# Kernel optimization log

Hardware: AMD Instinct MI355X
Metric: run time of the kernel (lower is better)

The kernel has to match this reference:

```python
import jax, jax.numpy as jnp
import numpy as np

D_MODEL = 512
WINDOW_SIZE = 257


def setup_inputs() -> dict:
    key = jax.random.key(0)
    ks = jax.random.split(key, 7)
    B, S, D = 4, 4096, D_MODEL
    scale = 1.0 / np.sqrt(D)
    return {
        "x": jax.random.normal(ks[0], (B, S, D), dtype=jnp.float32),
        "Wq": jax.random.normal(ks[1], (D, D), dtype=jnp.float32) * scale,
        "bq": jnp.zeros((D,), dtype=jnp.float32),
        "Wk": jax.random.normal(ks[2], (D, D), dtype=jnp.float32) * scale,
        "bk": jnp.zeros((D,), dtype=jnp.float32),
        "Wv": jax.random.normal(ks[3], (D, D), dtype=jnp.float32) * scale,
        "bv": jnp.zeros((D,), dtype=jnp.float32),
    }


def reference(x, Wq, bq, Wk, bk, Wv, bv):
    B, S, D = x.shape
    half_window = (WINDOW_SIZE - 1) // 2
    Q = x @ Wq + bq
    K = x @ Wk + bk
    V = x @ Wv + bv
    # full [B,S,S] scores, then band mask |i-j| <= half_window (matches original)
    scores = jnp.einsum("bsd,btd->bst", Q, K) / jnp.sqrt(jnp.asarray(D, x.dtype))
    idx = jnp.arange(S)
    local_mask = jnp.abs(idx[:, None] - idx[None, :]) <= half_window  # [S,S]
    scores = jnp.where(local_mask[None], scores, -jnp.inf)
    attn = jax.nn.softmax(scores, axis=-1)
    return jnp.einsum("bst,btd->bsd", attn, V)
```

## Files before the change

kernel.cpp:

```cpp
#include <hip/hip_runtime.h>
#include <hip/hip_bf16.h>

#define S_LEN   4096
#define D_MOD   512
#define BATCH   4
#define HALF_W  128
#define M_TOT   (BATCH * S_LEN)

typedef __attribute__((ext_vector_type(8))) short bf16x8;
typedef __attribute__((ext_vector_type(4))) float f32x4;

__device__ __forceinline__ unsigned short f2bf(float f) {
    unsigned int u = __float_as_uint(f);
    unsigned int r = (u + 0x7fffu + ((u >> 16) & 1u)) >> 16;
    return (unsigned short)r;
}

__device__ __forceinline__ void async_copy16(const void* g, void* l) {
    __builtin_amdgcn_global_load_lds(
        (const __attribute__((address_space(1))) void*)g,
        (__attribute__((address_space(3))) void*)l, 16, 0, 0);
}

__global__ __launch_bounds__(256) void convert_xw(const float* __restrict__ x,
                                                  const float* __restrict__ Wq,
                                                  const float* __restrict__ Wk,
                                                  const float* __restrict__ Wv,
                                                  unsigned short* __restrict__ xb,
                                                  unsigned short* __restrict__ Wt) {
    __shared__ float sT[64][65];
    const int t = threadIdx.x;
    const int bid = blockIdx.x;
    if (bid < 8192) {
        int i = (bid * 256 + t) * 4;
        float4 v = *(const float4*)(x + i);
        ushort4 o;
        o.x = f2bf(v.x); o.y = f2bf(v.y); o.z = f2bf(v.z); o.w = f2bf(v.w);
        *(ushort4*)(xb + i) = o;
        return;
    }
    const int j = bid - 8192;
    const int w = j >> 6;
    const int rj = j & 63;
    const float* W = (w == 0) ? Wq : ((w == 1) ? Wk : Wv);
    const int n0 = (rj & 7) * 64, k0 = (rj >> 3) * 64;
    const int r = t >> 4, c4 = (t & 15) * 4;
    #pragma unroll
    for (int i = 0; i < 4; ++i) {
        float4 v = *(const float4*)(W + (size_t)(k0 + r + i * 16) * 512 + n0 + c4);
        sT[c4 + 0][r + i * 16] = v.x;
        sT[c4 + 1][r + i * 16] = v.y;
        sT[c4 + 2][r + i * 16] = v.z;
        sT[c4 + 3][r + i * 16] = v.w;
    }
    __syncthreads();
    #pragma unroll
    for (int i = 0; i < 4; ++i) {
        int rr = (t >> 4) + i * 16;
        ushort4 o;
        o.x = f2bf(sT[rr][c4 + 0]);
        o.y = f2bf(sT[rr][c4 + 1]);
        o.z = f2bf(sT[rr][c4 + 2]);
        o.w = f2bf(sT[rr][c4 + 3]);
        *(ushort4*)(Wt + (size_t)w * 262144 + (size_t)(n0 + rr) * 512 + k0 + c4) = o;
    }
}

__global__ __launch_bounds__(256) void qkv_gemm(
    const unsigned short* __restrict__ xb, const unsigned short* __restrict__ Wt,
    const float* __restrict__ bq, const float* __restrict__ bk, const float* __restrict__ bv,
    unsigned short* __restrict__ Qo, unsigned short* __restrict__ Ko,
    unsigned short* __restrict__ Vt) {
    __shared__ __align__(16) char gsmem[34816];
    unsigned short* sA = (unsigned short*)gsmem;
    unsigned short* sB = (unsigned short*)(gsmem + 16384);
    unsigned short* sT = (unsigned short*)gsmem;

    const int t = threadIdx.x;
    const int p = blockIdx.x;
    const int l = (p & 7) * 192 + (p >> 3);
    const int mi = l / 12;
    const int rzn = l - mi * 12;
    const int wsel = rzn >> 2;
    const int ni = rzn & 3;
    const int m0 = mi * 128;
    const int n0 = ni * 128;
    const unsigned short* Wb = Wt + (size_t)wsel * 262144;

    const int w = t >> 6, lane = t & 63;
    const int wm = (w & 1) * 64, wn = (w >> 1) * 64;
    const int qd = lane >> 4, l16 = lane & 15;

    f32x4 acc[4][4] = {};

    for (int k0 = 0; k0 < 512; k0 += 64) {
        __syncthreads();
        #pragma unroll
        for (int i = 0; i < 4; ++i) {
            int c = i * 256 + t;
            int row = c >> 3, cc = c & 7;
            int g = cc ^ (row & 7);
            async_copy16(xb + (size_t)(m0 + row) * 512 + k0 + g * 8, sA + c * 8);
            async_copy16(Wb + (size_t)(n0 + row) * 512 + k0 + g * 8, sB + c * 8);
        }
        __syncthreads();
        #pragma unroll
        for (int ks = 0; ks < 2; ++ks) {
            bf16x8 af[4], bfr[4];
            #pragma unroll
            for (int i = 0; i < 4; ++i) {
                int row = wm + i * 16 + l16;
                int ch = (ks * 4 + qd) ^ (row & 7);
                af[i] = *(const bf16x8*)(sA + row * 64 + ch * 8);
            }
            #pragma unroll
            for (int j = 0; j < 4; ++j) {
                int row = wn + j * 16 + l16;
                int ch = (ks * 4 + qd) ^ (row & 7);
                bfr[j] = *(const bf16x8*)(sB + row * 64 + ch * 8);
            }
            #pragma unroll
            for (int i = 0; i < 4; ++i)
                #pragma unroll
                for (int j = 0; j < 4; ++j)
                    acc[i][j] = __builtin_amdgcn_mfma_f32_16x16x32_bf16(af[i], bfr[j], acc[i][j], 0, 0, 0);
        }
    }

    const float* bias = (wsel == 0) ? bq : ((wsel == 1) ? bk : bv);
    __syncthreads();

    if (wsel < 2) {
        #pragma unroll
        for (int j = 0; j < 4; ++j) {
            int n = wn + j * 16 + l16;
            float bj = bias[n0 + n];
            #pragma unroll
            for (int i = 0; i < 4; ++i) {
                int mb = wm + i * 16 + qd * 4;
                #pragma unroll
                for (int r = 0; r < 4; ++r)
                    sT[(mb + r) * 136 + n] = f2bf(acc[i][j][r] + bj);
            }
        }
        __syncthreads();
        unsigned short* Og = (wsel == 0) ? Qo : Ko;
        #pragma unroll
        for (int i2 = 0; i2 < 4; ++i2)
            #pragma unroll
            for (int i3 = 0; i3 < 2; ++i3) {
                int m = i2 * 32 + (t >> 3);
                int ch = (t & 7) + i3 * 8;
                bf16x8 v = *(const bf16x8*)(sT + m * 136 + ch * 8);
                *(bf16x8*)(Og + (size_t)(m0 + m) * 512 + n0 + ch * 8) = v;
            }
    } else {
        #pragma unroll
        for (int j = 0; j < 4; ++j) {
            int n = wn + j * 16 + l16;
            float bj = bias[n0 + n];
            #pragma unroll
            for (int i = 0; i < 4; ++i) {
                int mb = wm + i * 16 + qd * 4;
                #pragma unroll
                for (int r = 0; r < 4; ++r)
                    sT[n * 136 + mb + r] = f2bf(acc[i][j][r] + bj);
            }
        }
        __syncthreads();
        #pragma unroll
        for (int i2 = 0; i2 < 4; ++i2)
            #pragma unroll
            for (int i3 = 0; i3 < 2; ++i3) {
                int n = i2 * 32 + (t >> 3);
                int ch = (t & 7) + i3 * 8;
                bf16x8 v = *(const bf16x8*)(sT + n * 136 + ch * 8);
                *(bf16x8*)(Vt + (size_t)(n0 + n) * M_TOT + m0 + ch * 8) = v;
            }
    }
}

__global__ __launch_bounds__(256) void attn(const unsigned short* __restrict__ Qg,
                                            const unsigned short* __restrict__ Kg,
                                            const unsigned short* __restrict__ Vt,
                                            float* __restrict__ out) {
    __shared__ __align__(16) unsigned short sQ[32 * 520];
    __shared__ __align__(16) unsigned short sKV[32 * 520];
    __shared__ __align__(16) unsigned short sP[32 * 40];
    __shared__ float lsum[32];

    const int t = threadIdx.x;
    const int p = blockIdx.x;
    const int l = (p & 7) * 64 + (p >> 3);
    const int q0 = (l & 127) * 32;
    const int b = l >> 7;
    const int bS = b * S_LEN;
    const int w = t >> 6, lane = t & 63;
    const int qd = lane >> 4, l16 = lane & 15;
    const int qh = (w >> 1) * 16, kh = (w & 1) * 16;

    if (t < 32) lsum[t] = 0.f;

    #pragma unroll
    for (int i = 0; i < 8; ++i) {
        int c = i * 256 + t;
        int row = c >> 6, cc = c & 63;
        async_copy16(Qg + (bS + q0 + row) * 512 + cc * 8, sQ + row * 520 + cc * 8);
    }
    asm volatile("s_waitcnt vmcnt(0)" ::: "memory");

    const int kt_lo = (q0 < 128) ? ((128 - q0) >> 5) : 0;
    int kt_hi = (4192 - q0) >> 5;
    if (kt_hi > 8) kt_hi = 8;

    bf16x8 kreg[8], vreg[8];

    {
        int key0 = q0 - HALF_W + kt_lo * 32;
        #pragma unroll
        for (int i = 0; i < 8; ++i) {
            int c = i * 256 + t;
            int row = c >> 6, cc = c & 63;
            int rowg = key0 + row;
            rowg = (rowg < 0) ? 0 : ((rowg > S_LEN - 1) ? S_LEN - 1 : rowg);
            kreg[i] = *(const bf16x8*)(Kg + (size_t)(bS + rowg) * 512 + cc * 8);
        }
    }

    f32x4 oacc[16] = {};

    for (int kt = kt_lo; kt <= kt_hi; ++kt) {
        const int key0 = q0 - HALF_W + kt * 32;

        asm volatile("s_waitcnt lgkmcnt(0)" ::: "memory");
        __builtin_amdgcn_s_barrier();

        #pragma unroll
        for (int i = 0; i < 8; ++i) {
            int c = i * 256 + t;
            int row = c >> 6, cc = c & 63;
            *(bf16x8*)(sKV + row * 520 + cc * 8) = kreg[i];
        }

        #pragma unroll
        for (int i = 0; i < 8; ++i) {
            int c = i * 256 + t;
            int rp = c >> 3, chs = c & 7;
            int ch = chs ^ (rp & 7);
            int d = rp * 2 + (ch >> 2);
            int kc = ch & 3;
            int kk = key0 + kc * 8;
            int koff = (kk >= 0 && kk + 8 <= S_LEN) ? kk : 0;
            vreg[i] = *(const bf16x8*)(Vt + (size_t)d * M_TOT + bS + koff);
        }

        asm volatile("s_waitcnt lgkmcnt(0)" ::: "memory");
        __builtin_amdgcn_s_barrier();

        f32x4 sacc = {0.f, 0.f, 0.f, 0.f};
        #pragma unroll
        for (int c4 = 0; c4 < 4; ++c4) {
            #pragma unroll
            for (int kc = 0; kc < 4; ++kc) {
                bf16x8 aq  = *(const bf16x8*)(sQ  + (qh + l16) * 520 + c4 * 128 + kc * 32 + qd * 8);
                bf16x8 bk8 = *(const bf16x8*)(sKV + (kh + l16) * 520 + c4 * 128 + kc * 32 + qd * 8);
                sacc = __builtin_amdgcn_mfma_f32_16x16x32_bf16(aq, bk8, sacc, 0, 0, 0);
            }
        }

        const float scale = 0.04419417382415922f;
        #pragma unroll
        for (int r = 0; r < 4; ++r) {
            int qi = q0 + qh + qd * 4 + r;
            int kj = key0 + kh + l16;
            bool valid = (kj >= 0) && (kj < S_LEN) && (kj >= qi - HALF_W) && (kj <= qi + HALF_W);
            float p2 = valid ? __expf(sacc[r] * scale) : 0.f;
            sP[(qh + qd * 4 + r) * 40 + kh + l16] = f2bf(p2);
            float s = p2;
            s += __shfl_xor(s, 1);
            s += __shfl_xor(s, 2);
            s += __shfl_xor(s, 4);
            s += __shfl_xor(s, 8);
            if (l16 == 0) atomicAdd(&lsum[qh + qd * 4 + r], s);
        }

        asm volatile("s_waitcnt lgkmcnt(0)" ::: "memory");
        __builtin_amdgcn_s_barrier();

        #pragma unroll
        for (int i = 0; i < 8; ++i) {
            int c = i * 256 + t;
            *(bf16x8*)(sKV + c * 8) = vreg[i];
        }

        if (kt < kt_hi) {
            int key0n = key0 + 32;
            #pragma unroll
            for (int i = 0; i < 8; ++i) {
                int c = i * 256 + t;
                int row = c >> 6, cc = c & 63;
                int rowg = key0n + row;
                rowg = (rowg < 0) ? 0 : ((rowg > S_LEN - 1) ? S_LEN - 1 : rowg);
                kreg[i] = *(const bf16x8*)(Kg + (size_t)(bS + rowg) * 512 + cc * 8);
            }
        }

        asm volatile("s_waitcnt lgkmcnt(0)" ::: "memory");
        __builtin_amdgcn_s_barrier();

        #pragma unroll
        for (int c4 = 0; c4 < 4; ++c4) {
            #pragma unroll
            for (int qt = 0; qt < 2; ++qt) {
                bf16x8 ap = *(const bf16x8*)(sP + (qt * 16 + l16) * 40 + qd * 8);
                #pragma unroll
                for (int dt = 0; dt < 2; ++dt) {
                    int dv = c4 * 128 + w * 32 + dt * 16 + l16;
                    int rp = dv >> 1;
                    int chs = (((dv & 1) << 2) + qd) ^ (rp & 7);
                    bf16x8 bv8 = *(const bf16x8*)(sKV + rp * 64 + chs * 8);
                    oacc[c4 * 4 + qt * 2 + dt] =
                        __builtin_amdgcn_mfma_f32_16x16x32_bf16(ap, bv8, oacc[c4 * 4 + qt * 2 + dt], 0, 0, 0);
                }
            }
        }
    }

    asm volatile("s_waitcnt lgkmcnt(0)" ::: "memory");
    __builtin_amdgcn_s_barrier();

    float inv[2][4];
    #pragma unroll
    for (int qt = 0; qt < 2; ++qt)
        #pragma unroll
        for (int r = 0; r < 4; ++r)
            inv[qt][r] = 1.0f / lsum[qt * 16 + qd * 4 + r];

    #pragma unroll
    for (int c4 = 0; c4 < 4; ++c4)
        #pragma unroll
        for (int qt = 0; qt < 2; ++qt)
            #pragma unroll
            for (int dt = 0; dt < 2; ++dt) {
                int dv = c4 * 128 + w * 32 + dt * 16 + l16;
                #pragma unroll
                for (int r = 0; r < 4; ++r) {
                    int q = qt * 16 + qd * 4 + r;
                    out[(size_t)(bS + q0 + q) * 512 + dv] = oacc[c4 * 4 + qt * 2 + dt][r] * inv[qt][r];
                }
            }
}

extern "C" void kernel_launch(void* const* d_in, const int* in_sizes, int n_in,
                              void* d_out, int out_size, void* d_ws, size_t ws_size,
                              hipStream_t stream) {
    const float* x  = (const float*)d_in[0];
    const float* Wq = (const float*)d_in[1];
    const float* bq = (const float*)d_in[2];
    const float* Wk = (const float*)d_in[3];
    const float* bk = (const float*)d_in[4];
    const float* Wv = (const float*)d_in[5];
    const float* bv = (const float*)d_in[6];
    float* out = (float*)d_out;

    char* ws = (char*)d_ws;
    unsigned short* xb = (unsigned short*)(ws);
    unsigned short* Wt = (unsigned short*)(ws + 16777216);
    unsigned short* Qb = (unsigned short*)(ws + 18350080);
    unsigned short* Kb = (unsigned short*)(ws + 35127296);
    unsigned short* Vt = (unsigned short*)(ws + 51904512);

    convert_xw<<<8384, 256, 0, stream>>>(x, Wq, Wk, Wv, xb, Wt);
    qkv_gemm<<<1536, 256, 0, stream>>>(xb, Wt, bq, bk, bv, Qb, Kb, Vt);
    attn<<<512, 256, 0, stream>>>(Qb, Kb, Vt, out);
}
```

Measured before the change: 165.1 us.

## Warp-specialize attention into QK-softmax and PV groups with pipelined tiles

The attention kernel grows to 512 threads. Four waves load K, compute QK^T and the exponentials, while the other four waves load V and run the P·V MFMAs on the previous key tile, using a double-buffered P buffer. Q is staged once through LDS into registers so QK^T no longer re-reads Q from shared memory, and K and V get separate LDS buffers. This aims to overlap the score and output phases and cut per-tile barriers, at the cost of higher register pressure under launch_bounds(512,2), which could spill, and an extra drain iteration per block.

```diff
diff --git a/kernel.cpp b/kernel.cpp
--- a/kernel.cpp
+++ b/kernel.cpp
@@ -180,13 +180,13 @@
     }
 }
 
-__global__ __launch_bounds__(256) void attn(const unsigned short* __restrict__ Qg,
-                                            const unsigned short* __restrict__ Kg,
-                                            const unsigned short* __restrict__ Vt,
-                                            float* __restrict__ out) {
-    __shared__ __align__(16) unsigned short sQ[32 * 520];
-    __shared__ __align__(16) unsigned short sKV[32 * 520];
-    __shared__ __align__(16) unsigned short sP[32 * 40];
+__global__ __launch_bounds__(512, 2) void attn(const unsigned short* __restrict__ Qg,
+                                               const unsigned short* __restrict__ Kg,
+                                               const unsigned short* __restrict__ Vt,
+                                               float* __restrict__ out) {
+    __shared__ __align__(16) unsigned short sK[32 * 520];
+    __shared__ __align__(16) unsigned short sV[32 * 512];
+    __shared__ __align__(16) unsigned short sP[2][32 * 40];
     __shared__ float lsum[32];
 
     const int t = threadIdx.x;
@@ -195,160 +195,192 @@
     const int q0 = (l & 127) * 32;
     const int b = l >> 7;
     const int bS = b * S_LEN;
-    const int w = t >> 6, lane = t & 63;
+
+    const bool isA = (t < 256);
+    const int ta = t & 255;
+    const int w = (t >> 6) & 3;
+    const int lane = t & 63;
     const int qd = lane >> 4, l16 = lane & 15;
     const int qh = (w >> 1) * 16, kh = (w & 1) * 16;
 
     if (t < 32) lsum[t] = 0.f;
-
-    #pragma unroll
-    for (int i = 0; i < 8; ++i) {
-        int c = i * 256 + t;
-        int row = c >> 6, cc = c & 63;
-        async_copy16(Qg + (bS + q0 + row) * 512 + cc * 8, sQ + row * 520 + cc * 8);
-    }
-    asm volatile("s_waitcnt vmcnt(0)" ::: "memory");
 
     const int kt_lo = (q0 < 128) ? ((128 - q0) >> 5) : 0;
     int kt_hi = (4192 - q0) >> 5;
     if (kt_hi > 8) kt_hi = 8;
 
-    bf16x8 kreg[8], vreg[8];
+    bf16x8 kreg[8], vreg[8], qreg[16];
+    f32x4 oacc[16] = {};
 
     {
         int key0 = q0 - HALF_W + kt_lo * 32;
-        #pragma unroll
-        for (int i = 0; i < 8; ++i) {
-            int c = i * 256 + t;
-            int row = c >> 6, cc = c & 63;
-            int rowg = key0 + row;
-            rowg = (rowg < 0) ? 0 : ((rowg > S_LEN - 1) ? S_LEN - 1 : rowg);
-            kreg[i] = *(const bf16x8*)(Kg + (size_t)(bS + rowg) * 512 + cc * 8);
-        }
-    }
-
-    f32x4 oacc[16] = {};
-
-    for (int kt = kt_lo; kt <= kt_hi; ++kt) {
+        if (isA) {
+            #pragma unroll
+            for (int i = 0; i < 8; ++i) {
+                int c = i * 256 + ta;
+                int row = c >> 6, cc = c & 63;
+                int rowg = key0 + row;
+                rowg = (rowg < 0) ? 0 : ((rowg > S_LEN - 1) ? S_LEN - 1 : rowg);
+                kreg[i] = *(const bf16x8*)(Kg + (size_t)(bS + rowg) * 512 + cc * 8);
+            }
+        } else {
+            #pragma unroll
+            for (int i = 0; i < 8; ++i) {
+                int c = i * 256 + ta;
+                int rp = c >> 3, chs = c & 7;
+                int ch = chs ^ (rp & 7);
+                int d = rp * 2 + (ch >> 2);
+                int kc = ch & 3;
+                int kk = key0 + kc * 8;
+                int koff = (kk >= 0 && kk + 8 <= S_LEN) ? kk : 0;
+                vreg[i] = *(const bf16x8*)(Vt + (size_t)d * M_TOT + bS + koff);
+            }
+        }
+    }
+
+    #pragma unroll
+    for (int i = 0; i < 4; ++i) {
+        int c = i * 512 + t;
+        int row = c >> 6, cc = c & 63;
+        async_copy16(Qg + (size_t)(bS + q0 + row) * 512 + cc * 8, sK + row * 512 + cc * 8);
+    }
+    asm volatile("s_waitcnt vmcnt(0)" ::: "memory");
+    __builtin_amdgcn_s_barrier();
+    if (isA) {
+        #pragma unroll
+        for (int c4 = 0; c4 < 4; ++c4)
+            #pragma unroll
+            for (int kc = 0; kc < 4; ++kc)
+                qreg[c4 * 4 + kc] = *(const bf16x8*)(sK + (qh + l16) * 512 + c4 * 128 + kc * 32 + qd * 8);
+    }
+    asm volatile("s_waitcnt lgkmcnt(0)" ::: "memory");
+    __builtin_amdgcn_s_barrier();
+
+    for (int kt = kt_lo; kt <= kt_hi + 1; ++kt) {
         const int key0 = q0 - HALF_W + kt * 32;
+
+        if (isA) {
+            if (kt <= kt_hi) {
+                #pragma unroll
+                for (int i = 0; i < 8; ++i) {
+                    int c = i * 256 + ta;
+                    int row = c >> 6, cc = c & 63;
+                    *(bf16x8*)(sK + row * 520 + cc * 8) = kreg[i];
+                }
+                if (kt < kt_hi) {
+                    int key0n = key0 + 32;
+                    #pragma unroll
+                    for (int i = 0; i < 8; ++i) {
+                        int c = i * 256 + ta;
+                        int row = c >> 6, cc = c & 63;
+                        int rowg = key0n + row;
+                        rowg = (rowg < 0) ? 0 : ((rowg > S_LEN - 1) ? S_LEN - 1 : rowg);
+                        kreg[i] = *(const bf16x8*)(Kg + (size_t)(bS + rowg) * 512 + cc * 8);
+                    }
+                }
+            }
+        } else {
+            if (kt > kt_lo) {
+                #pragma unroll
+                for (int i = 0; i < 8; ++i) {
+                    int c = i * 256 + ta;
+                    *(bf16x8*)(sV + c * 8) = vreg[i];
+                }
+            }
+            if (kt > kt_lo && kt <= kt_hi) {
+                #pragma unroll
+                for (int i = 0; i < 8; ++i) {
+                    int c = i * 256 + ta;
+                    int rp = c >> 3, chs = c & 7;
+                    int ch = chs ^ (rp & 7);
+                    int d = rp * 2 + (ch >> 2);
+                    int kc = ch & 3;
+                    int kk = key0 + kc * 8;
+                    int koff = (kk >= 0 && kk + 8 <= S_LEN) ? kk : 0;
+                    vreg[i] = *(const bf16x8*)(Vt + (size_t)d * M_TOT + bS + koff);
+                }
+            }
+        }
 
         asm volatile("s_waitcnt lgkmcnt(0)" ::: "memory");
         __builtin_amdgcn_s_barrier();
 
-        #pragma unroll
-        for (int i = 0; i < 8; ++i) {
-            int c = i * 256 + t;
-            int row = c >> 6, cc = c & 63;
-            *(bf16x8*)(sKV + row * 520 + cc * 8) = kreg[i];
-        }
-
-        #pragma unroll
-        for (int i = 0; i < 8; ++i) {
-            int c = i * 256 + t;
-            int rp = c >> 3, chs = c & 7;
-            int ch = chs ^ (rp & 7);
-            int d = rp * 2 + (ch >> 2);
-            int kc = ch & 3;
-            int kk = key0 + kc * 8;
-            int koff = (kk >= 0 && kk + 8 <= S_LEN) ? kk : 0;
-            vreg[i] = *(const bf16x8*)(Vt + (size_t)d * M_TOT + bS + koff);
+        if (isA) {
+            if (kt <= kt_hi) {
+                f32x4 sacc = {0.f, 0.f, 0.f, 0.f};
+                #pragma unroll
+                for (int c4 = 0; c4 < 4; ++c4) {
+                    #pragma unroll
+                    for (int kc = 0; kc < 4; ++kc) {
+                        bf16x8 bk8 = *(const bf16x8*)(sK + (kh + l16) * 520 + c4 * 128 + kc * 32 + qd * 8);
+                        sacc = __builtin_amdgcn_mfma_f32_16x16x32_bf16(qreg[c4 * 4 + kc], bk8, sacc, 0, 0, 0);
+                    }
+                }
+                const float scale = 0.04419417382415922f;
+                unsigned short* sPt = sP[kt & 1];
+                #pragma unroll
+                for (int r = 0; r < 4; ++r) {
+                    int qi = q0 + qh + qd * 4 + r;
+                    int kj = key0 + kh + l16;
+                    bool valid = (kj >= 0) && (kj < S_LEN) && (kj >= qi - HALF_W) && (kj <= qi + HALF_W);
+                    float p2 = valid ? __expf(sacc[r] * scale) : 0.f;
+                    sPt[(qh + qd * 4 + r) * 40 + kh + l16] = f2bf(p2);
+                    float s = p2;
+                    s += __shfl_xor(s, 1);
+                    s += __shfl_xor(s, 2);
+                    s += __shfl_xor(s, 4);
+                    s += __shfl_xor(s, 8);
+                    if (l16 == 0) atomicAdd(&lsum[qh + qd * 4 + r], s);
+                }
+            }
+        } else {
+            if (kt > kt_lo) {
+                const unsigned short* sPp = sP[(kt - 1) & 1];
+                #pragma unroll
+                for (int c4 = 0; c4 < 4; ++c4) {
+                    #pragma unroll
+                    for (int qt = 0; qt < 2; ++qt) {
+                        bf16x8 ap = *(const bf16x8*)(sPp + (qt * 16 + l16) * 40 + qd * 8);
+                        #pragma unroll
+                        for (int dt = 0; dt < 2; ++dt) {
+                            int dv = c4 * 128 + w * 32 + dt * 16 + l16;
+                            int rp = dv >> 1;
+                            int chs = (((dv & 1) << 2) + qd) ^ (rp & 7);
+                            bf16x8 bv8 = *(const bf16x8*)(sV + rp * 64 + chs * 8);
+                            oacc[c4 * 4 + qt * 2 + dt] =
+                                __builtin_amdgcn_mfma_f32_16x16x32_bf16(ap, bv8, oacc[c4 * 4 + qt * 2 + dt], 0, 0, 0);
+                        }
+                    }
+                }
+            }
         }
 
         asm volatile("s_waitcnt lgkmcnt(0)" ::: "memory");
         __builtin_amdgcn_s_barrier();
-
-        f32x4 sacc = {0.f, 0.f, 0.f, 0.f};
-        #pragma unroll
-        for (int c4 = 0; c4 < 4; ++c4) {
-            #pragma unroll
-            for (int kc = 0; kc < 4; ++kc) {
-                bf16x8 aq  = *(const bf16x8*)(sQ  + (qh + l16) * 520 + c4 * 128 + kc * 32 + qd * 8);
-                bf16x8 bk8 = *(const bf16x8*)(sKV + (kh + l16) * 520 + c4 * 128 + kc * 32 + qd * 8);
-                sacc = __builtin_amdgcn_mfma_f32_16x16x32_bf16(aq, bk8, sacc, 0, 0, 0);
-            }
-        }
-
-        const float scale = 0.04419417382415922f;
-        #pragma unroll
-        for (int r = 0; r < 4; ++r) {
-            int qi = q0 + qh + qd * 4 + r;
-            int kj = key0 + kh + l16;
-            bool valid = (kj >= 0) && (kj < S_LEN) && (kj >= qi - HALF_W) && (kj <= qi + HALF_W);
-            float p2 = valid ? __expf(sacc[r] * scale) : 0.f;
-            sP[(qh + qd * 4 + r) * 40 + kh + l16] = f2bf(p2);
-            float s = p2;
-            s += __shfl_xor(s, 1);
-            s += __shfl_xor(s, 2);
-            s += __shfl_xor(s, 4);
-            s += __shfl_xor(s, 8);
-            if (l16 == 0) atomicAdd(&lsum[qh + qd * 4 + r], s);
-        }
-
-        asm volatile("s_waitcnt lgkmcnt(0)" ::: "memory");
-        __builtin_amdgcn_s_barrier();
-
-        #pragma unroll
-        for (int i = 0; i < 8; ++i) {
-            int c = i * 256 + t;
-            *(bf16x8*)(sKV + c * 8) = vreg[i];
-        }
-
-        if (kt < kt_hi) {
-            int key0n = key0 + 32;
-            #pragma unroll
-            for (int i = 0; i < 8; ++i) {
-                int c = i * 256 + t;
-                int row = c >> 6, cc = c & 63;
-                int rowg = key0n + row;
-                rowg = (rowg < 0) ? 0 : ((rowg > S_LEN - 1) ? S_LEN - 1 : rowg);
-                kreg[i] = *(const bf16x8*)(Kg + (size_t)(bS + rowg) * 512 + cc * 8);
-            }
-        }
-
-        asm volatile("s_waitcnt lgkmcnt(0)" ::: "memory");
-        __builtin_amdgcn_s_barrier();
-
-        #pragma unroll
-        for (int c4 = 0; c4 < 4; ++c4) {
-            #pragma unroll
-            for (int qt = 0; qt < 2; ++qt) {
-                bf16x8 ap = *(const bf16x8*)(sP + (qt * 16 + l16) * 40 + qd * 8);
+    }
+
+    if (!isA) {
+        float inv[2][4];
+        #pragma unroll
+        for (int qt = 0; qt < 2; ++qt)
+            #pragma unroll
+            for (int r = 0; r < 4; ++r)
+                inv[qt][r] = 1.0f / lsum[qt * 16 + qd * 4 + r];
+
+        #pragma unroll
+        for (int c4 = 0; c4 < 4; ++c4)
+            #pragma unroll
+            for (int qt = 0; qt < 2; ++qt)
                 #pragma unroll
                 for (int dt = 0; dt < 2; ++dt) {
                     int dv = c4 * 128 + w * 32 + dt * 16 + l16;
-                    int rp = dv >> 1;
-                    int chs = (((dv & 1) << 2) + qd) ^ (rp & 7);
-                    bf16x8 bv8 = *(const bf16x8*)(sKV + rp * 64 + chs * 8);
-                    oacc[c4 * 4 + qt * 2 + dt] =
-                        __builtin_amdgcn_mfma_f32_16x16x32_bf16(ap, bv8, oacc[c4 * 4 + qt * 2 + dt], 0, 0, 0);
-                }
-            }
-        }
-    }
-
-    asm volatile("s_waitcnt lgkmcnt(0)" ::: "memory");
-    __builtin_amdgcn_s_barrier();
-
-    float inv[2][4];
-    #pragma unroll
-    for (int qt = 0; qt < 2; ++qt)
-        #pragma unroll
-        for (int r = 0; r < 4; ++r)
-            inv[qt][r] = 1.0f / lsum[qt * 16 + qd * 4 + r];
-
-    #pragma unroll
-    for (int c4 = 0; c4 < 4; ++c4)
-        #pragma unroll
-        for (int qt = 0; qt < 2; ++qt)
-            #pragma unroll
-            for (int dt = 0; dt < 2; ++dt) {
-                int dv = c4 * 128 + w * 32 + dt * 16 + l16;
-                #pragma unroll
-                for (int r = 0; r < 4; ++r) {
-                    int q = qt * 16 + qd * 4 + r;
-                    out[(size_t)(bS + q0 + q) * 512 + dv] = oacc[c4 * 4 + qt * 2 + dt][r] * inv[qt][r];
-                }
-            }
+                    #pragma unroll
+                    for (int r = 0; r < 4; ++r) {
+                        int q = qt * 16 + qd * 4 + r;
+                        out[(size_t)(bS + q0 + q) * 512 + dv] = oacc[c4 * 4 + qt * 2 + dt][r] * inv[qt][r];
+                    }
+                }
+    }
 }
 
 extern "C" void kernel_launch(void* const* d_in, const int* in_sizes, int n_in,
@@ -372,5 +404,5 @@
 
     convert_xw<<<8384, 256, 0, stream>>>(x, Wq, Wk, Wv, xb, Wt);
     qkv_gemm<<<1536, 256, 0, stream>>>(xb, Wt, bq, bk, bv, Qb, Kb, Vt);
-    attn<<<512, 256, 0, stream>>>(Qb, Kb, Vt, out);
-}
+    attn<<<512, 512, 0, stream>>>(Qb, Kb, Vt, out);
+}
```

After: 199.9 us. 1.21x slower.

## Double-buffer K/V tiles via async LDS loads with 64-query, 512-thread blocks

Applied to the files above, without the earlier changes.

The attention kernel moves to 64-query tiles processed by 512 threads. K and V tiles are fetched straight into LDS with global_load_lds and double-buffered, so the next tile's loads overlap the current tile's MFMAs. Q fragments are loaded once into registers from a swizzled LDS copy, which removes the repeated Q LDS reads. The block now uses about 134KB of LDS and 256 blocks, which lowers occupancy and grid parallelism and processes one extra key tile per block.

```diff
diff --git a/kernel.cpp b/kernel.cpp
--- a/kernel.cpp
+++ b/kernel.cpp
@@ -180,94 +180,128 @@
     }
 }
 
-__global__ __launch_bounds__(256) void attn(const unsigned short* __restrict__ Qg,
-                                            const unsigned short* __restrict__ Kg,
-                                            const unsigned short* __restrict__ Vt,
-                                            float* __restrict__ out) {
-    __shared__ __align__(16) unsigned short sQ[32 * 520];
-    __shared__ __align__(16) unsigned short sKV[32 * 520];
-    __shared__ __align__(16) unsigned short sP[32 * 40];
-    __shared__ float lsum[32];
+__global__ __launch_bounds__(512, 2) void attn(const unsigned short* __restrict__ Qg,
+                                               const unsigned short* __restrict__ Kg,
+                                               const unsigned short* __restrict__ Vt,
+                                               float* __restrict__ out) {
+    __shared__ __align__(16) char smem[137472];
+    unsigned short* const bK0 = (unsigned short*)(smem);
+    unsigned short* const bK1 = (unsigned short*)(smem + 66048);
+    unsigned short* const bV0 = (unsigned short*)(smem + 33280);
+    unsigned short* const bV1 = (unsigned short*)(smem + 99328);
+    unsigned short* const sQ  = (unsigned short*)(smem + 66048);
+    unsigned short* const sP  = (unsigned short*)(smem + 132096);
+    float* const lsum = (float*)(smem + 137216);
 
     const int t = threadIdx.x;
     const int p = blockIdx.x;
-    const int l = (p & 7) * 64 + (p >> 3);
-    const int q0 = (l & 127) * 32;
-    const int b = l >> 7;
+    const int l = (p & 7) * 32 + (p >> 3);
+    const int q0 = (l & 63) * 64;
+    const int b = l >> 6;
     const int bS = b * S_LEN;
+
     const int w = t >> 6, lane = t & 63;
     const int qd = lane >> 4, l16 = lane & 15;
-    const int qh = (w >> 1) * 16, kh = (w & 1) * 16;
-
-    if (t < 32) lsum[t] = 0.f;
-
-    #pragma unroll
-    for (int i = 0; i < 8; ++i) {
-        int c = i * 256 + t;
-        int row = c >> 6, cc = c & 63;
-        async_copy16(Qg + (bS + q0 + row) * 512 + cc * 8, sQ + row * 520 + cc * 8);
-    }
-    asm volatile("s_waitcnt vmcnt(0)" ::: "memory");
+    const int qs = w >> 1;
+    const int qh = qs * 16;
+    const int kh = (w & 1) * 16;
+    const int dh = (w & 1) * 256;
+
+    if (t < 64) lsum[t] = 0.f;
 
     const int kt_lo = (q0 < 128) ? ((128 - q0) >> 5) : 0;
     int kt_hi = (4192 - q0) >> 5;
-    if (kt_hi > 8) kt_hi = 8;
-
-    bf16x8 kreg[8], vreg[8];
+    if (kt_hi > 9) kt_hi = 9;
+
+    bf16x8 qreg[16];
+    f32x4 oacc[16] = {};
 
     {
         int key0 = q0 - HALF_W + kt_lo * 32;
         #pragma unroll
-        for (int i = 0; i < 8; ++i) {
-            int c = i * 256 + t;
+        for (int i = 0; i < 4; ++i) {
+            int c = i * 512 + t;
             int row = c >> 6, cc = c & 63;
             int rowg = key0 + row;
             rowg = (rowg < 0) ? 0 : ((rowg > S_LEN - 1) ? S_LEN - 1 : rowg);
-            kreg[i] = *(const bf16x8*)(Kg + (size_t)(bS + rowg) * 512 + cc * 8);
-        }
-    }
-
-    f32x4 oacc[16] = {};
-
-    for (int kt = kt_lo; kt <= kt_hi; ++kt) {
-        const int key0 = q0 - HALF_W + kt * 32;
-
-        asm volatile("s_waitcnt lgkmcnt(0)" ::: "memory");
-        __builtin_amdgcn_s_barrier();
-
-        #pragma unroll
-        for (int i = 0; i < 8; ++i) {
-            int c = i * 256 + t;
-            int row = c >> 6, cc = c & 63;
-            *(bf16x8*)(sKV + row * 520 + cc * 8) = kreg[i];
-        }
-
-        #pragma unroll
-        for (int i = 0; i < 8; ++i) {
-            int c = i * 256 + t;
+            async_copy16(Kg + (size_t)(bS + rowg) * 512 + cc * 8, bK0 + row * 520 + cc * 8);
+        }
+        #pragma unroll
+        for (int i = 0; i < 4; ++i) {
+            int c = i * 512 + t;
             int rp = c >> 3, chs = c & 7;
             int ch = chs ^ (rp & 7);
             int d = rp * 2 + (ch >> 2);
             int kc = ch & 3;
             int kk = key0 + kc * 8;
             int koff = (kk >= 0 && kk + 8 <= S_LEN) ? kk : 0;
-            vreg[i] = *(const bf16x8*)(Vt + (size_t)d * M_TOT + bS + koff);
-        }
-
-        asm volatile("s_waitcnt lgkmcnt(0)" ::: "memory");
+            async_copy16(Vt + (size_t)d * M_TOT + bS + koff, bV0 + c * 8);
+        }
+        #pragma unroll
+        for (int i = 0; i < 8; ++i) {
+            int c = i * 512 + t;
+            int row = c >> 6, cc = c & 63;
+            int g = cc ^ (row & 7);
+            async_copy16(Qg + (size_t)(bS + q0 + row) * 512 + g * 8, sQ + row * 512 + cc * 8);
+        }
+    }
+    asm volatile("s_waitcnt vmcnt(0)" ::: "memory");
+    __builtin_amdgcn_s_barrier();
+    #pragma unroll
+    for (int c4 = 0; c4 < 4; ++c4)
+        #pragma unroll
+        for (int kc = 0; kc < 4; ++kc) {
+            int chl = c4 * 16 + kc * 4 + qd;
+            int chp = chl ^ (l16 & 7);
+            qreg[c4 * 4 + kc] = *(const bf16x8*)(sQ + (qh + l16) * 512 + chp * 8);
+        }
+    asm volatile("s_waitcnt lgkmcnt(0)" ::: "memory");
+    __builtin_amdgcn_s_barrier();
+
+    int cur = 0;
+    for (int kt = kt_lo; kt <= kt_hi; ++kt, cur ^= 1) {
+        const int key0 = q0 - HALF_W + kt * 32;
+
+        asm volatile("s_waitcnt vmcnt(0) lgkmcnt(0)" ::: "memory");
         __builtin_amdgcn_s_barrier();
 
+        if (kt < kt_hi) {
+            int key0n = key0 + 32;
+            unsigned short* dK = cur ? bK0 : bK1;
+            unsigned short* dV = cur ? bV0 : bV1;
+            #pragma unroll
+            for (int i = 0; i < 4; ++i) {
+                int c = i * 512 + t;
+                int row = c >> 6, cc = c & 63;
+                int rowg = key0n + row;
+                rowg = (rowg < 0) ? 0 : ((rowg > S_LEN - 1) ? S_LEN - 1 : rowg);
+                async_copy16(Kg + (size_t)(bS + rowg) * 512 + cc * 8, dK + row * 520 + cc * 8);
+            }
+            #pragma unroll
+            for (int i = 0; i < 4; ++i) {
+                int c = i * 512 + t;
+                int rp = c >> 3, chs = c & 7;
+                int ch = chs ^ (rp & 7);
+                int d = rp * 2 + (ch >> 2);
+                int kc = ch & 3;
+                int kk = key0n + kc * 8;
+                int koff = (kk >= 0 && kk + 8 <= S_LEN) ? kk : 0;
+                async_copy16(Vt + (size_t)d * M_TOT + bS + koff, dV + c * 8);
+            }
+        }
+
+        const unsigned short* sK = cur ? bK1 : bK0;
+        const unsigned short* sV = cur ? bV1 : bV0;
+
         f32x4 sacc = {0.f, 0.f, 0.f, 0.f};
         #pragma unroll
         for (int c4 = 0; c4 < 4; ++c4) {
             #pragma unroll
             for (int kc = 0; kc < 4; ++kc) {
-                bf16x8 aq  = *(const bf16x8*)(sQ  + (qh + l16) * 520 + c4 * 128 + kc * 32 + qd * 8);
-                bf16x8 bk8 = *(const bf16x8*)(sKV + (kh + l16) * 520 + c4 * 128 + kc * 32 + qd * 8);
-                sacc = __builtin_amdgcn_mfma_f32_16x16x32_bf16(aq, bk8, sacc, 0, 0, 0);
-            }
-        }
-
+                bf16x8 bk8 = *(const bf16x8*)(sK + (kh + l16) * 520 + c4 * 128 + kc * 32 + qd * 8);
+                sacc = __builtin_amdgcn_mfma_f32_16x16x32_bf16(qreg[c4 * 4 + kc], bk8, sacc, 0, 0, 0);
+            }
+        }
         const float scale = 0.04419417382415922f;
         #pragma unroll
         for (int r = 0; r < 4; ++r) {
@@ -287,68 +321,34 @@
         asm volatile("s_waitcnt lgkmcnt(0)" ::: "memory");
         __builtin_amdgcn_s_barrier();
 
-        #pragma unroll
-        for (int i = 0; i < 8; ++i) {
-            int c = i * 256 + t;
-            *(bf16x8*)(sKV + c * 8) = vreg[i];
-        }
-
-        if (kt < kt_hi) {
-            int key0n = key0 + 32;
-            #pragma unroll
-            for (int i = 0; i < 8; ++i) {
-                int c = i * 256 + t;
-                int row = c >> 6, cc = c & 63;
-                int rowg = key0n + row;
-                rowg = (rowg < 0) ? 0 : ((rowg > S_LEN - 1) ? S_LEN - 1 : rowg);
-                kreg[i] = *(const bf16x8*)(Kg + (size_t)(bS + rowg) * 512 + cc * 8);
-            }
-        }
-
-        asm volatile("s_waitcnt lgkmcnt(0)" ::: "memory");
-        __builtin_amdgcn_s_barrier();
-
-        #pragma unroll
-        for (int c4 = 0; c4 < 4; ++c4) {
-            #pragma unroll
-            for (int qt = 0; qt < 2; ++qt) {
-                bf16x8 ap = *(const bf16x8*)(sP + (qt * 16 + l16) * 40 + qd * 8);
-                #pragma unroll
-                for (int dt = 0; dt < 2; ++dt) {
-                    int dv = c4 * 128 + w * 32 + dt * 16 + l16;
-                    int rp = dv >> 1;
-                    int chs = (((dv & 1) << 2) + qd) ^ (rp & 7);
-                    bf16x8 bv8 = *(const bf16x8*)(sKV + rp * 64 + chs * 8);
-                    oacc[c4 * 4 + qt * 2 + dt] =
-                        __builtin_amdgcn_mfma_f32_16x16x32_bf16(ap, bv8, oacc[c4 * 4 + qt * 2 + dt], 0, 0, 0);
-                }
-            }
+        bf16x8 ap = *(const bf16x8*)(sP + (qh + l16) * 40 + qd * 8);
+        #pragma unroll
+        for (int dt = 0; dt < 16; ++dt) {
+            int dv = dh + dt * 16 + l16;
+            int rp = dv >> 1;
+            int chs = (((dv & 1) << 2) + qd) ^ (rp & 7);
+            bf16x8 bv8 = *(const bf16x8*)(sV + rp * 64 + chs * 8);
+            oacc[dt] = __builtin_amdgcn_mfma_f32_16x16x32_bf16(ap, bv8, oacc[dt], 0, 0, 0);
         }
     }
 
     asm volatile("s_waitcnt lgkmcnt(0)" ::: "memory");
     __builtin_amdgcn_s_barrier();
 
-    float inv[2][4];
-    #pragma unroll
-    for (int qt = 0; qt < 2; ++qt)
-        #pragma unroll
-        for (int r = 0; r < 4; ++r)
-            inv[qt][r] = 1.0f / lsum[qt * 16 + qd * 4 + r];
-
-    #pragma unroll
-    for (int c4 = 0; c4 < 4; ++c4)
-        #pragma unroll
-        for (int qt = 0; qt < 2; ++qt)
-            #pragma unroll
-            for (int dt = 0; dt < 2; ++dt) {
-                int dv = c4 * 128 + w * 32 + dt * 16 + l16;
-                #pragma unroll
-                for (int r = 0; r < 4; ++r) {
-                    int q = qt * 16 + qd * 4 + r;
-                    out[(size_t)(bS + q0 + q) * 512 + dv] = oacc[c4 * 4 + qt * 2 + dt][r] * inv[qt][r];
-                }
-            }
+    float inv[4];
+    #pragma unroll
+    for (int r = 0; r < 4; ++r)
+        inv[r] = 1.0f / lsum[qh + qd * 4 + r];
+
+    #pragma unroll
+    for (int dt = 0; dt < 16; ++dt) {
+        int dv = dh + dt * 16 + l16;
+        #pragma unroll
+        for (int r = 0; r < 4; ++r) {
+            int q = qh + qd * 4 + r;
+            out[(size_t)(bS + q0 + q) * 512 + dv] = oacc[dt][r] * inv[r];
+        }
+    }
 }
 
 extern "C" void kernel_launch(void* const* d_in, const int* in_sizes, int n_in,
@@ -372,5 +372,5 @@
 
     convert_xw<<<8384, 256, 0, stream>>>(x, Wq, Wk, Wv, xb, Wt);
     qkv_gemm<<<1536, 256, 0, stream>>>(xb, Wt, bq, bk, bv, Qb, Kb, Vt);
-    attn<<<512, 256, 0, stream>>>(Qb, Kb, Vt, out);
-}
+    attn<<<256, 512, 0, stream>>>(Qb, Kb, Vt, out);
+}
```

Result: no change. 163.7 us (-0.8%).
